# Kernel optimization log

Hardware: AMD Instinct MI355X
Metric: run time of the kernel (lower is better)

The kernel has to match this reference:

```python
import jax, jax.numpy as jnp
import numpy as np

A_NUM = 9
C_NUM = 20

def setup_inputs() -> dict:
    key = jax.random.key(0)
    ks = jax.random.split(key, 12)
    B, Cin, H, W = 32, 256, 56, 56
    hidden = 256
    N, M = 64, 2048
    out_ch = 5 * A_NUM + C_NUM
    features = jax.random.normal(ks[0], (B, Cin, H, W), jnp.float32)
    w1 = jax.random.normal(ks[1], (hidden, Cin), jnp.float32) * (1.0 / np.sqrt(Cin))
    b1 = jax.random.normal(ks[2], (hidden,), jnp.float32) * 0.01
    w2 = jax.random.normal(ks[3], (out_ch, hidden), jnp.float32) * (1.0 / np.sqrt(hidden))
    b2 = jax.random.normal(ks[4], (out_ch,), jnp.float32) * 0.01
    # anchor shapes (w, h), positive sizes in grid units
    anc = 1.0 + 5.0 * jax.random.uniform(ks[5], (A_NUM, 2), jnp.float32)
    # grid of cell centers
    xs = jnp.arange(W, dtype=jnp.float32) + 0.5
    ys = jnp.arange(H, dtype=jnp.float32) + 0.5
    gx, gy = jnp.meshgrid(xs, ys, indexing='xy')  # (H, W)
    grid = jnp.broadcast_to(jnp.stack([gx, gy], axis=-1)[None], (B, H, W, 2))
    # GT boxes (x1, y1, x2, y2, cls) with x1<x2, y1<y2
    x1 = jax.random.uniform(ks[6], (B, N), jnp.float32) * (W - 9.0)
    y1 = jax.random.uniform(ks[7], (B, N), jnp.float32) * (H - 9.0)
    bw = 1.0 + 7.0 * jax.random.uniform(ks[8], (B, N), jnp.float32)
    bh = 1.0 + 7.0 * jax.random.uniform(ks[9], (B, N), jnp.float32)
    cls = jax.random.randint(ks[10], (B, N), 0, C_NUM).astype(jnp.float32)
    bboxes = jnp.stack([x1, y1, x1 + bw, y1 + bh, cls], axis=-1)
    total_anchors = B * A_NUM * H * W
    pos_anchor_idx = jax.random.randint(ks[11], (M,), 0, total_anchors, jnp.int64 if jax.config.jax_enable_x64 else jnp.int32)
    neg_anchor_idx = jax.random.randint(jax.random.fold_in(key, 99), (M,), 0, total_anchors, jnp.int64 if jax.config.jax_enable_x64 else jnp.int32)
    GT_offsets = jax.random.normal(jax.random.fold_in(key, 100), (M, 4), jnp.float32) * 0.1
    return {"features": features, "w1": w1, "b1": b1, "w2": w2, "b2": b2,
            "anc": anc, "grid": grid, "bboxes": bboxes, "GT_offsets": GT_offsets,
            "pos_anchor_idx": pos_anchor_idx, "neg_anchor_idx": neg_anchor_idx}

def _generate_anchor(anc, grid):
    # grid: (B,H,W,2), anc: (A,2) -> anchors (B,A,H,W,4) as (x1,y1,x2,y2)
    g = grid[:, None]                      # (B,1,H,W,2)
    a = anc[None, :, None, None]           # (1,A,1,1,2)
    return jnp.concatenate([g - a / 2, g + a / 2], axis=-1)

def _generate_proposal_yolo(anchors, offsets):
    ctr = (anchors[..., :2] + anchors[..., 2:]) / 2
    wh = anchors[..., 2:] - anchors[..., :2]
    new_wh = wh * jnp.exp(offsets[..., 2:])
    new_ctr = ctr + offsets[..., :2]
    return jnp.concatenate([new_ctr - new_wh / 2, new_ctr + new_wh / 2], axis=-1)

def _iou(proposals, bboxes):
    # proposals (B,A,H,W,4) -> (B,AHW,4); bboxes (B,N,5) -> iou (B,AHW,N)
    B = proposals.shape[0]
    p = proposals.reshape(B, -1, 4)[:, :, None, :]   # (B,AHW,1,4)
    g = bboxes[:, None, :, :]                        # (B,1,N,5)
    ix1 = jnp.maximum(p[..., 0], g[..., 0])
    iy1 = jnp.maximum(p[..., 1], g[..., 1])
    ix2 = jnp.minimum(p[..., 2], g[..., 2])
    iy2 = jnp.minimum(p[..., 3], g[..., 3])
    inter = jnp.clip(ix2 - ix1, 0) * jnp.clip(iy2 - iy1, 0)
    gt_area = (bboxes[:, :, 2] - bboxes[:, :, 0]) * (bboxes[:, :, 3] - bboxes[:, :, 1])
    p_area = (p[..., 2] - p[..., 0]) * (p[..., 3] - p[..., 1])
    return inter / (gt_area[:, None, :] + p_area - inter)

def reference(features, w1, b1, w2, b2, anc, grid, bboxes, GT_offsets,
              pos_anchor_idx, neg_anchor_idx):
    B, _, H, W = features.shape
    A = anc.shape[0]
    M = pos_anchor_idx.shape[0]
    # PredictionNetwork (dropout in eval = identity), 1x1 convs as einsum
    x = jnp.einsum('bchw,oc->bohw', features, w1) + b1[None, :, None, None]
    x = jax.nn.leaky_relu(x, 0.01)
    x = jnp.einsum('bchw,oc->bohw', x, w2) + b2[None, :, None, None]
    anc_data = x[:, :5 * A].reshape(B, A, 5, H, W)
    class_all = x[:, 5 * A:]                               # (B,C,H,W)
    conf_all = jax.nn.sigmoid(anc_data[:, :, 0])           # (B,A,H,W)
    offsets_all = jnp.transpose(anc_data[:, :, 1:5], (0, 1, 3, 4, 2))  # (B,A,H,W,4)
    # training extraction
    conf_flat = conf_all.reshape(-1)
    conf_scores = jnp.concatenate([conf_flat[pos_anchor_idx], conf_flat[neg_anchor_idx]])[:, None]  # (2M,1)
    offsets_pos = offsets_all.reshape(-1, 4)[pos_anchor_idx]            # (M,4)
    # class scores for positive anchors: index arithmetic over (B,A,H,W)
    bi = pos_anchor_idx // (A * H * W)
    hw = pos_anchor_idx % (H * W)
    hi, wi = hw // W, hw % W
    class_pos = class_all[bi, :, hi, wi]                                # (M,C)
    # anchors -> proposals -> IoU
    anchors = _generate_anchor(anc, grid)
    proposals = _generate_proposal_yolo(anchors, offsets_all)
    iou_mat = _iou(proposals, bboxes)                                   # (B,AHW,N)
    # YOLO SSE losses
    gt_conf = jnp.concatenate([jnp.ones((M, 1), conf_scores.dtype), jnp.zeros((M, 1), conf_scores.dtype)])
    conf_loss = jnp.sum((conf_scores - gt_conf) ** 2) / (2 * M)
    reg_loss = jnp.sum((offsets_pos - GT_offsets) ** 2) / M
    total_loss = conf_loss + reg_loss
    return total_loss, iou_mat, class_pos
```

## Files before the change

kernel.cpp:

```cpp
#include <hip/hip_runtime.h>
#include <math.h>

#define B_    32
#define CIN   256
#define HID   256
#define OC    65
#define A_    9
#define H_    56
#define W_    56
#define HW    3136
#define AHW   28224
#define NBOX  64
#define M_    2048
#define CNUM  20
#define NTILE 49

#define IOU_N ((size_t)B_ * AHW * NBOX)
#define X2_BYTES ((size_t)B_ * OC * HW * 4)

#define FOFF(frag) (((frag) << 3) + ((((frag) >> 3)) << 3))

typedef _Float16 half8 __attribute__((ext_vector_type(8)));
typedef float f32x16 __attribute__((ext_vector_type(16)));
typedef float f32x4  __attribute__((ext_vector_type(4)));

__device__ __forceinline__ unsigned int pkh(float a, float b) {
    _Float16 ha = (_Float16)a, hb = (_Float16)b;
    unsigned short ua = __builtin_bit_cast(unsigned short, ha);
    unsigned short ub = __builtin_bit_cast(unsigned short, hb);
    return (unsigned int)ua | ((unsigned int)ub << 16);
}

__global__ __launch_bounds__(256) void prep_kernel(
    const float* __restrict__ w1, const float* __restrict__ w2,
    _Float16* __restrict__ w1s, _Float16* __restrict__ w2s)
{
    const int f = blockIdx.x * 256 + threadIdx.x;
    {
        const int e    = f & 7;
        const int lane = (f >> 3) & 63;
        const int kc   = (f >> 9) & 15;
        const int ob   = f >> 13;
        const int row  = ob * 32 + (lane & 31);
        const int k    = kc * 16 + (lane >> 5) * 8 + e;
        w1s[f] = (_Float16)w1[row * CIN + k];
    }
    if (f < 20480) {
        const int e    = f & 7;
        const int lane = (f >> 3) & 63;
        const int ks2  = (f >> 9) & 7;
        const int rt   = f >> 12;
        const int row  = rt * 16 + (lane & 15);
        const int k    = ks2 * 32 + (lane >> 4) * 8 + e;
        w2s[f] = (row < OC) ? (_Float16)w2[row * HID + k] : (_Float16)0.f;
    }
}

__global__ __launch_bounds__(256) void conv_iou_kernel(
    const float* __restrict__ features, const _Float16* __restrict__ w1s,
    const float* __restrict__ b1, const _Float16* __restrict__ w2s,
    const float* __restrict__ b2, const float* __restrict__ anc,
    const float* __restrict__ bboxes, float* __restrict__ x2,
    float* __restrict__ iou_out)
{
    __shared__ _Float16 lds_h[18432];
    __shared__ float bias_s[HID];
    __shared__ float boxs[5 * 64];

    _Float16* featAll = lds_h;
    _Float16* hidf    = lds_h;
    float*    L       = (float*)lds_h;
    float*    x2t     = L;
    float*    ppx1    = L + 4416;
    float*    ppy1    = L + 4992;
    float*    ppx2    = L + 5568;
    float*    ppy2    = L + 6144;
    float*    pare    = L + 6720;

    const int t    = threadIdx.x;
    const int lane = t & 63;
    const int w    = t >> 6;
    const int bid  = blockIdx.x;
    const int b    = bid / NTILE;
    const int p0   = (bid - b * NTILE) * 64;
    const float* fbase = features + (size_t)b * CIN * HW + p0;

    bias_s[t] = b1[t];
    if (t < 64) {
        const float* gb = bboxes + ((size_t)b * NBOX + t) * 5;
        const float x1 = gb[0], y1 = gb[1], x2v = gb[2], y2v = gb[3];
        boxs[t] = x1; boxs[64 + t] = y1; boxs[128 + t] = x2v; boxs[192 + t] = y2v;
        boxs[256 + t] = (x2v - x1) * (y2v - y1);
    }

    const int pstage = (t & 15) * 4;
    const int kk     = (t >> 4) * 2;
    const int ksS    = kk >> 4;
    const int gS     = (kk >> 3) & 1;
    const int j0h    = kk & 7;
    const int ghalf  = lane >> 5;

#pragma unroll
    for (int c = 0; c < 8; ++c) {
        const float4 r0 = *(const float4*)(fbase + (size_t)(c * 32 + kk) * HW + pstage);
        const float4 r1 = *(const float4*)(fbase + (size_t)(c * 32 + kk + 1) * HW + pstage);
        const float a0[4] = {r0.x, r0.y, r0.z, r0.w};
        const float a1[4] = {r1.x, r1.y, r1.z, r1.w};
#pragma unroll
        for (int e = 0; e < 4; ++e) {
            const int p     = pstage + e;
            const int lane2 = gS * 32 + (p & 31);
            const int pt    = p >> 5;
            const int frag  = c * 256 + (ksS * 2 + pt) * 64 + lane2;
            *(unsigned int*)&featAll[FOFF(frag) + j0h] = pkh(a0[e], a1[e]);
        }
    }
    __syncthreads();

    f32x16 facc[2][2];
#pragma unroll
    for (int ot = 0; ot < 2; ++ot)
#pragma unroll
        for (int pt = 0; pt < 2; ++pt)
#pragma unroll
            for (int e = 0; e < 16; ++e) facc[ot][pt][e] = 0.f;

    half8 afb[2][2][2];
#pragma unroll
    for (int ks = 0; ks < 2; ++ks)
#pragma unroll
        for (int ot = 0; ot < 2; ++ot)
            afb[0][ks][ot] = *(const half8*)(w1s + ((size_t)((w * 2 + ot) * 16 + ks) * 64 + lane) * 8);

#pragma unroll
    for (int c = 0; c < 8; ++c) {
        if (c < 7) {
#pragma unroll
            for (int ks = 0; ks < 2; ++ks)
#pragma unroll
                for (int ot = 0; ot < 2; ++ot)
                    afb[(c + 1) & 1][ks][ot] =
                        *(const half8*)(w1s + ((size_t)((w * 2 + ot) * 16 + (c + 1) * 2 + ks) * 64 + lane) * 8);
        }
#pragma unroll
        for (int ks = 0; ks < 2; ++ks) {
#pragma unroll
            for (int pt = 0; pt < 2; ++pt) {
                const half8 bf = *(const half8*)&featAll[FOFF(c * 256 + (ks * 2 + pt) * 64 + lane)];
                facc[0][pt] = __builtin_amdgcn_mfma_f32_32x32x16_f16(afb[c & 1][ks][0], bf, facc[0][pt], 0, 0, 0);
                facc[1][pt] = __builtin_amdgcn_mfma_f32_32x32x16_f16(afb[c & 1][ks][1], bf, facc[1][pt], 0, 0, 0);
            }
        }
    }
    __syncthreads();

    const int col = lane & 31;
#pragma unroll
    for (int ot = 0; ot < 2; ++ot) {
        const int ks2 = w * 2 + ot;
#pragma unroll
        for (int pt = 0; pt < 2; ++pt) {
            const int pt2 = pt * 2 + (col >> 4);
            const int n15 = col & 15;
#pragma unroll
            for (int q = 0; q < 4; ++q) {
                float hv[4];
#pragma unroll
                for (int i = 0; i < 4; ++i) {
                    const int row = i + 8 * q + 4 * ghalf;
                    float v = facc[ot][pt][q * 4 + i] + bias_s[w * 64 + ot * 32 + row];
                    hv[i] = v < 0.f ? 0.01f * v : v;
                }
                const int frag = (ks2 * 4 + pt2) * 64 + (q * 16 + n15);
                *(unsigned int*)&hidf[FOFF(frag) + 4 * ghalf]     = pkh(hv[0], hv[1]);
                *(unsigned int*)&hidf[FOFF(frag) + 4 * ghalf + 2] = pkh(hv[2], hv[3]);
            }
        }
    }
    __syncthreads();

    f32x4 c2[5];
#pragma unroll
    for (int rt = 0; rt < 5; ++rt)
#pragma unroll
        for (int e = 0; e < 4; ++e) c2[rt][e] = 0.f;

    const int m16 = lane & 15;
    const int kgr = lane >> 4;
#pragma unroll 2
    for (int ks2 = 0; ks2 < 8; ++ks2) {
        const half8 bf = *(const half8*)&hidf[FOFF((ks2 * 4 + w) * 64 + lane)];
#pragma unroll
        for (int rt = 0; rt < 5; ++rt) {
            const half8 af = *(const half8*)(w2s + ((size_t)(rt * 8 + ks2) * 64 + lane) * 8);
            c2[rt] = __builtin_amdgcn_mfma_f32_16x16x32_f16(af, bf, c2[rt], 0, 0, 0);
        }
    }
    __syncthreads();

    float* xb = x2 + (size_t)b * OC * HW + p0 + w * 16 + m16;
    const int pxl = w * 16 + m16;
#pragma unroll
    for (int rt = 0; rt < 5; ++rt) {
#pragma unroll
        for (int r = 0; r < 4; ++r) {
            const int o2 = rt * 16 + kgr * 4 + r;
            const float v = c2[rt][r] + b2[o2];
            if (o2 < OC) {
                xb[(size_t)o2 * HW] = v;
                x2t[pxl * 69 + o2] = v;
            }
        }
    }
    __syncthreads();

    for (int pi = t; pi < A_ * 64; pi += 256) {
        const int a  = pi >> 6;
        const int px = pi & 63;
        const float* xr = x2t + px * 69 + 5 * a;
        const float tx = xr[1], ty = xr[2], tw = xr[3], th = xr[4];
        const int hw = p0 + px;
        const int h  = hw / W_;
        const int wv = hw - h * W_;
        const float gx = (float)wv + 0.5f;
        const float gy = (float)h + 0.5f;
        const float nw = anc[2 * a]     * __expf(tw);
        const float nh = anc[2 * a + 1] * __expf(th);
        const float cx = gx + tx, cy = gy + ty;
        ppx1[pi] = cx - 0.5f * nw; ppy1[pi] = cy - 0.5f * nh;
        ppx2[pi] = cx + 0.5f * nw; ppy2[pi] = cy + 0.5f * nh;
        pare[pi] = nw * nh;
    }
    __syncthreads();

    const int pr = lane >> 4;
    const int j0 = (lane & 15) * 4;
    float Bx1[4], By1[4], Bx2[4], By2[4], Ba[4];
#pragma unroll
    for (int e = 0; e < 4; ++e) {
        Bx1[e] = boxs[j0 + e];       By1[e] = boxs[64 + j0 + e];
        Bx2[e] = boxs[128 + j0 + e]; By2[e] = boxs[192 + j0 + e];
        Ba[e]  = boxs[256 + j0 + e];
    }
    float* ibase = iou_out + ((size_t)b * AHW + p0) * 64;
#pragma unroll 1
    for (int a = 0; a < A_; ++a) {
#pragma unroll
        for (int q = 0; q < 4; ++q) {
            const int p = w * 16 + q * 4 + pr;
            const int i = a * 64 + p;
            const float Px1 = ppx1[i], Py1 = ppy1[i], Px2 = ppx2[i], Py2 = ppy2[i];
            const float pa = pare[i];
            f32x4 o4;
#pragma unroll
            for (int e = 0; e < 4; ++e) {
                const float iw = fminf(Px2, Bx2[e]) - fmaxf(Px1, Bx1[e]);
                const float ih = fminf(Py2, By2[e]) - fmaxf(Py1, By1[e]);
                const float inter = fmaxf(iw, 0.f) * fmaxf(ih, 0.f);
                o4[e] = inter * __builtin_amdgcn_rcpf(Ba[e] + pa - inter);
            }
            __builtin_nontemporal_store(o4, (f32x4*)(ibase + ((size_t)a * HW + p) * 64 + j0));
        }
    }
}

__global__ __launch_bounds__(1024) void tail_kernel(
    const float* __restrict__ x2, const int* __restrict__ pos_idx,
    const int* __restrict__ neg_idx, const float* __restrict__ gt_off,
    float* __restrict__ cls_out, float* __restrict__ out0)
{
    const int t = threadIdx.x;
    if (blockIdx.x < 40) {
        const int g = blockIdx.x * 1024 + t;
        const int m = g / CNUM;
        const int c = g - m * CNUM;
        const int idx = pos_idx[m];
        const int bi  = idx / AHW;
        const int hw  = idx % HW;
        cls_out[g] = x2[((size_t)bi * OC + 45 + c) * HW + hw];
        return;
    }
    float csum = 0.f, rsum = 0.f;
    for (int m = t; m < M_; m += 1024) {
        const int idx = pos_idx[m];
        const int bi = idx / AHW;
        const int rr = idx - bi * AHW;
        const int a  = rr / HW;
        const int hw = rr - a * HW;
        const float* xb = x2 + ((size_t)bi * OC + 5 * a) * HW + hw;
        const float s = 1.f / (1.f + __expf(-xb[0]));
        csum += (s - 1.f) * (s - 1.f);
#pragma unroll
        for (int k = 0; k < 4; ++k) {
            const float d = xb[(size_t)(k + 1) * HW] - gt_off[m * 4 + k];
            rsum += d * d;
        }
    }
    for (int m = t; m < M_; m += 1024) {
        const int idx = neg_idx[m];
        const int bi = idx / AHW;
        const int rr = idx - bi * AHW;
        const int a  = rr / HW;
        const int hw = rr - a * HW;
        const float s = 1.f / (1.f + __expf(-x2[((size_t)bi * OC + 5 * a) * HW + hw]));
        csum += s * s;
    }
    __shared__ float red[32];
#pragma unroll
    for (int off = 32; off > 0; off >>= 1) {
        csum += __shfl_down(csum, off, 64);
        rsum += __shfl_down(rsum, off, 64);
    }
    if ((t & 63) == 0) { red[t >> 6] = csum; red[16 + (t >> 6)] = rsum; }
    __syncthreads();
    if (t == 0) {
        float c = 0.f, rg = 0.f;
#pragma unroll
        for (int i = 0; i < 16; ++i) { c += red[i]; rg += red[16 + i]; }
        out0[0] = c / (2.f * (float)M_) + rg / (float)M_;
    }
}

extern "C" void kernel_launch(void* const* d_in, const int* in_sizes, int n_in,
                              void* d_out, int out_size, void* d_ws, size_t ws_size,
                              hipStream_t stream) {
    (void)in_sizes; (void)n_in; (void)out_size; (void)ws_size;
    const float* features = (const float*)d_in[0];
    const float* w1       = (const float*)d_in[1];
    const float* b1       = (const float*)d_in[2];
    const float* w2       = (const float*)d_in[3];
    const float* b2       = (const float*)d_in[4];
    const float* anc      = (const float*)d_in[5];
    const float* bboxes   = (const float*)d_in[7];
    const float* gt_off   = (const float*)d_in[8];
    const int*   pos_idx  = (const int*)d_in[9];
    const int*   neg_idx  = (const int*)d_in[10];
    float* out = (float*)d_out;

    char* wsb = (char*)d_ws;
    float* x2 = (float*)wsb;
    _Float16* w1s = (_Float16*)(wsb + X2_BYTES);
    _Float16* w2s = w1s + 65536;

    prep_kernel<<<256, 256, 0, stream>>>(w1, w2, w1s, w2s);
    conv_iou_kernel<<<B_ * NTILE, 256, 0, stream>>>(features, w1s, b1, w2s, b2,
                                                    anc, bboxes, x2, out + 1);
    tail_kernel<<<41, 1024, 0, stream>>>(x2, pos_idx, neg_idx, gt_off, out + 1 + IOU_N, out);
}
```

Baseline: 386.6 us.

## Fuse loss and class gather into conv kernel, drop x2 global buffer

Removes the global x2 intermediate. Each conv tile now scans the pos/neg index lists and, for indices that fall in its own 64-pixel tile, computes the loss terms and writes class scores straight from LDS, accumulating the loss sums with atomics. A one-thread finalize kernel replaces the tail kernel. This saves the x2 write and the scattered re-reads, but every one of the 1568 blocks now scans all 4096 indices, and float atomics make the summation order nondeterministic.

Measured after the change: 379.1 us. No clear change (-1.9%).

```diff
diff --git a/kernel.cpp b/kernel.cpp
--- a/kernel.cpp
+++ b/kernel.cpp
@@ -16,7 +16,6 @@
 #define NTILE 49
 
 #define IOU_N ((size_t)B_ * AHW * NBOX)
-#define X2_BYTES ((size_t)B_ * OC * HW * 4)
 
 #define FOFF(frag) (((frag) << 3) + ((((frag) >> 3)) << 3))
 
@@ -33,9 +32,11 @@
 
 __global__ __launch_bounds__(256) void prep_kernel(
     const float* __restrict__ w1, const float* __restrict__ w2,
-    _Float16* __restrict__ w1s, _Float16* __restrict__ w2s)
+    _Float16* __restrict__ w1s, _Float16* __restrict__ w2s,
+    float* __restrict__ loss_ws)
 {
     const int f = blockIdx.x * 256 + threadIdx.x;
+    if (f < 2) loss_ws[f] = 0.f;
     {
         const int e    = f & 7;
         const int lane = (f >> 3) & 63;
@@ -60,12 +61,15 @@
     const float* __restrict__ features, const _Float16* __restrict__ w1s,
     const float* __restrict__ b1, const _Float16* __restrict__ w2s,
     const float* __restrict__ b2, const float* __restrict__ anc,
-    const float* __restrict__ bboxes, float* __restrict__ x2,
-    float* __restrict__ iou_out)
+    const float* __restrict__ bboxes, const int* __restrict__ pos_idx,
+    const int* __restrict__ neg_idx, const float* __restrict__ gt_off,
+    float* __restrict__ iou_out, float* __restrict__ cls_out,
+    float* __restrict__ loss_ws)
 {
     __shared__ _Float16 lds_h[18432];
     __shared__ float bias_s[HID];
     __shared__ float boxs[5 * 64];
+    __shared__ float red[8];
 
     _Float16* featAll = lds_h;
     _Float16* hidf    = lds_h;
@@ -198,18 +202,13 @@
     }
     __syncthreads();
 
-    float* xb = x2 + (size_t)b * OC * HW + p0 + w * 16 + m16;
     const int pxl = w * 16 + m16;
 #pragma unroll
     for (int rt = 0; rt < 5; ++rt) {
 #pragma unroll
         for (int r = 0; r < 4; ++r) {
             const int o2 = rt * 16 + kgr * 4 + r;
-            const float v = c2[rt][r] + b2[o2];
-            if (o2 < OC) {
-                xb[(size_t)o2 * HW] = v;
-                x2t[pxl * 69 + o2] = v;
-            }
+            if (o2 < OC) x2t[pxl * 69 + o2] = c2[rt][r] + b2[o2];
         }
     }
     __syncthreads();
@@ -262,63 +261,59 @@
             __builtin_nontemporal_store(o4, (f32x4*)(ibase + ((size_t)a * HW + p) * 64 + j0));
         }
     }
-}
-
-__global__ __launch_bounds__(1024) void tail_kernel(
-    const float* __restrict__ x2, const int* __restrict__ pos_idx,
-    const int* __restrict__ neg_idx, const float* __restrict__ gt_off,
-    float* __restrict__ cls_out, float* __restrict__ out0)
-{
-    const int t = threadIdx.x;
-    if (blockIdx.x < 40) {
-        const int g = blockIdx.x * 1024 + t;
-        const int m = g / CNUM;
-        const int c = g - m * CNUM;
+
+    float csum = 0.f, rsum = 0.f;
+    for (int m = t; m < M_; m += 256) {
         const int idx = pos_idx[m];
         const int bi  = idx / AHW;
-        const int hw  = idx % HW;
-        cls_out[g] = x2[((size_t)bi * OC + 45 + c) * HW + hw];
-        return;
-    }
-    float csum = 0.f, rsum = 0.f;
-    for (int m = t; m < M_; m += 1024) {
-        const int idx = pos_idx[m];
-        const int bi = idx / AHW;
-        const int rr = idx - bi * AHW;
-        const int a  = rr / HW;
-        const int hw = rr - a * HW;
-        const float* xb = x2 + ((size_t)bi * OC + 5 * a) * HW + hw;
-        const float s = 1.f / (1.f + __expf(-xb[0]));
-        csum += (s - 1.f) * (s - 1.f);
-#pragma unroll
-        for (int k = 0; k < 4; ++k) {
-            const float d = xb[(size_t)(k + 1) * HW] - gt_off[m * 4 + k];
-            rsum += d * d;
-        }
-    }
-    for (int m = t; m < M_; m += 1024) {
+        const int rr  = idx - bi * AHW;
+        const int a   = rr / HW;
+        const int px  = (rr - a * HW) - p0;
+        if (bi == b && px >= 0 && px < 64) {
+            const float* xr = x2t + px * 69;
+            const float s = 1.f / (1.f + __expf(-xr[5 * a]));
+            csum += (s - 1.f) * (s - 1.f);
+#pragma unroll
+            for (int k = 0; k < 4; ++k) {
+                const float d = xr[5 * a + 1 + k] - gt_off[m * 4 + k];
+                rsum += d * d;
+            }
+            float* co = cls_out + (size_t)m * CNUM;
+#pragma unroll
+            for (int c = 0; c < CNUM; ++c) co[c] = xr[45 + c];
+        }
+    }
+    for (int m = t; m < M_; m += 256) {
         const int idx = neg_idx[m];
-        const int bi = idx / AHW;
-        const int rr = idx - bi * AHW;
-        const int a  = rr / HW;
-        const int hw = rr - a * HW;
-        const float s = 1.f / (1.f + __expf(-x2[((size_t)bi * OC + 5 * a) * HW + hw]));
-        csum += s * s;
-    }
-    __shared__ float red[32];
+        const int bi  = idx / AHW;
+        const int rr  = idx - bi * AHW;
+        const int a   = rr / HW;
+        const int px  = (rr - a * HW) - p0;
+        if (bi == b && px >= 0 && px < 64) {
+            const float s = 1.f / (1.f + __expf(-x2t[px * 69 + 5 * a]));
+            csum += s * s;
+        }
+    }
 #pragma unroll
     for (int off = 32; off > 0; off >>= 1) {
         csum += __shfl_down(csum, off, 64);
         rsum += __shfl_down(rsum, off, 64);
     }
-    if ((t & 63) == 0) { red[t >> 6] = csum; red[16 + (t >> 6)] = rsum; }
+    if (lane == 0) { red[w] = csum; red[4 + w] = rsum; }
     __syncthreads();
     if (t == 0) {
-        float c = 0.f, rg = 0.f;
-#pragma unroll
-        for (int i = 0; i < 16; ++i) { c += red[i]; rg += red[16 + i]; }
-        out0[0] = c / (2.f * (float)M_) + rg / (float)M_;
-    }
+        const float c  = red[0] + red[1] + red[2] + red[3];
+        const float rg = red[4] + red[5] + red[6] + red[7];
+        if (c != 0.f || rg != 0.f) {
+            atomicAdd(&loss_ws[0], c);
+            atomicAdd(&loss_ws[1], rg);
+        }
+    }
+}
+
+__global__ void finalize_kernel(const float* __restrict__ loss_ws, float* __restrict__ out0)
+{
+    out0[0] = loss_ws[0] / (2.f * (float)M_) + loss_ws[1] / (float)M_;
 }
 
 extern "C" void kernel_launch(void* const* d_in, const int* in_sizes, int n_in,
@@ -338,12 +333,14 @@
     float* out = (float*)d_out;
 
     char* wsb = (char*)d_ws;
-    float* x2 = (float*)wsb;
-    _Float16* w1s = (_Float16*)(wsb + X2_BYTES);
-    _Float16* w2s = w1s + 65536;
-
-    prep_kernel<<<256, 256, 0, stream>>>(w1, w2, w1s, w2s);
+    _Float16* w1s  = (_Float16*)wsb;
+    _Float16* w2s  = w1s + 65536;
+    float* loss_ws = (float*)(wsb + 131072 + 40960);
+
+    prep_kernel<<<256, 256, 0, stream>>>(w1, w2, w1s, w2s, loss_ws);
     conv_iou_kernel<<<B_ * NTILE, 256, 0, stream>>>(features, w1s, b1, w2s, b2,
-                                                    anc, bboxes, x2, out + 1);
-    tail_kernel<<<41, 1024, 0, stream>>>(x2, pos_idx, neg_idx, gt_off, out + 1 + IOU_N, out);
-}
+                                                    anc, bboxes, pos_idx, neg_idx,
+                                                    gt_off, out + 1,
+                                                    out + 1 + IOU_N, loss_ws);
+    finalize_kernel<<<1, 1, 0, stream>>>(loss_ws, out);
+}
```
